# Optimization experiments

Measured on AMD Instinct MI355X. Metric: run time of the kernel, lower is better.

Reference implementation:

```python
import jax, jax.numpy as jnp
import numpy as np

N_HEAD, D_K, D_V, D_MODEL, D_OUT = 8, 64, 64, 512, 512
TOP_K = 5 + 1  # Sparse_attention.__init__ does top_k += 1
EPS = 1e-7
TEMPERATURE = float(np.power(D_K, 0.5))


def setup_inputs() -> dict:
    key = jax.random.key(0)
    ks = jax.random.split(key, 13)
    B, LQ, LK = 4, 1024, 1024
    f32 = jnp.float32
    std_qk = float(np.sqrt(2.0 / (D_MODEL + D_K)))
    std_v = float(np.sqrt(2.0 / (D_MODEL + D_V)))
    std_fc = float(np.sqrt(2.0 / (N_HEAD * D_V + D_OUT)))  # xavier normal
    return {
        "q": jax.random.normal(ks[0], (B, LQ, D_MODEL), f32),
        "k": jax.random.normal(ks[1], (B, LK, D_MODEL), f32),
        "v": jax.random.normal(ks[2], (B, LK, D_MODEL), f32),
        "Wq": jax.random.normal(ks[3], (N_HEAD * D_K, D_MODEL), f32) * std_qk,
        "bq": jax.random.normal(ks[4], (N_HEAD * D_K,), f32) * 0.01,
        "Wk": jax.random.normal(ks[5], (N_HEAD * D_K, D_MODEL), f32) * std_qk,
        "bk": jax.random.normal(ks[6], (N_HEAD * D_K,), f32) * 0.01,
        "Wv": jax.random.normal(ks[7], (N_HEAD * D_V, D_MODEL), f32) * std_v,
        "bv": jax.random.normal(ks[8], (N_HEAD * D_V,), f32) * 0.01,
        "Wfc": jax.random.normal(ks[9], (D_OUT, N_HEAD * D_V), f32) * std_fc,
        "bfc": jax.random.normal(ks[10], (D_OUT,), f32) * 0.01,
        "Wg": jaxax_norm if False else jax.random.normal(ks[11], (D_OUT, N_HEAD * D_V), f32) * std_fc,
        "bg": jax.random.normal(ks[12], (D_OUT,), f32) * 0.01,
    }


def _sparse_attention(attn):
    # attn: (bh, lq, lk) softmax weights; keep values >= TOP_K-th largest per row
    # (time_step = lk > TOP_K always here, so only the else-branch applies)
    delta = jax.lax.top_k(attn, TOP_K)[0][..., -1:] + EPS  # (bh, lq, 1)
    w = jnp.maximum(attn - delta, 0.0)
    return w / (jnp.sum(w, axis=-1, keepdims=True) + EPS)


def reference(q, k, v, Wq, bq, Wk, bk, Wv, bv, Wfc, bfc, Wg, bg):
    B, LQ, _ = q.shape
    LK = k.shape[1]
    # QKV projections, split heads, head-major flatten (matches permute(2,0,1,3))
    qh = (q @ Wq.T + bq).reshape(B, LQ, N_HEAD, D_K)
    kh = (k @ Wk.T + bk).reshape(B, LK, N_HEAD, D_K)
    vh = (v @ Wv.T + bv).reshape(B, LK, N_HEAD, D_V)
    qh = jnp.transpose(qh, (2, 0, 1, 3)).reshape(N_HEAD * B, LQ, D_K)
    kh = jnp.transpose(kh, (2, 0, 1, 3)).reshape(N_HEAD * B, LK, D_K)
    vh = jnp.transpose(vh, (2, 0, 1, 3)).reshape(N_HEAD * B, LK, D_V)
    scores = jnp.einsum("bqd,bkd->bqk", qh, kh) / TEMPERATURE
    attn = jax.nn.softmax(scores, axis=-1)
    attn = _sparse_attention(attn)
    out = jnp.einsum("bqk,bkd->bqd", attn, vh)  # (h*B, lq, d_v)
    out = out.reshape(N_HEAD, B, LQ, D_V)
    out = jnp.transpose(out, (1, 2, 0, 3)).reshape(B, LQ, N_HEAD * D_V)
    # dropout is identity in eval mode
    fc_out = out @ Wfc.T + bfc
    gate = jax.nn.sigmoid(out @ Wg.T + bg)
    output = gate * jnp.tanh(fc_out)
    return output, attn
```

## Files before the change

kernel.cpp:

```cpp
#include <hip/hip_runtime.h>
#include <hip/hip_bf16.h>
#include <math.h>

#define SEQ    1024
#define DMODEL 512
#define OUT0   2097152
#define SP_EPS 1e-7f
#define INV_T  0.125f

typedef __attribute__((ext_vector_type(8))) short bf16x8;
typedef __attribute__((ext_vector_type(4))) float f32x4;

__device__ __forceinline__ unsigned short f2bf(float f) {
  unsigned int b = __float_as_uint(f);
  return (unsigned short)((b + 0x7fffu + ((b >> 16) & 1u)) >> 16);
}
__device__ __forceinline__ float bf2f(unsigned short u) {
  return __uint_as_float(((unsigned int)u) << 16);
}

__device__ __forceinline__ float wred_max(float v) {
#pragma unroll
  for (int o = 32; o > 0; o >>= 1) v = fmaxf(v, __shfl_xor(v, o));
  return v;
}
__device__ __forceinline__ float wred_sum(float v) {
#pragma unroll
  for (int o = 32; o > 0; o >>= 1) v += __shfl_xor(v, o);
  return v;
}

__global__ __launch_bounds__(256) void convW_kernel(
    const float* __restrict__ w0, const float* __restrict__ w1,
    const float* __restrict__ w2, unsigned short* __restrict__ dst)
{
  const int z = blockIdx.z;
  const float* src = (z == 0) ? w0 : (z == 1) ? w1 : w2;
  unsigned short* hi = dst + (size_t)z * (1u << 19);
  unsigned short* lo = hi + (1u << 18);
  const int i = (blockIdx.x * 256 + threadIdx.x) * 4;
  const float4 x = *(const float4*)(src + i);
  ushort4 h, l;
  h.x = f2bf(x.x); l.x = f2bf(x.x - bf2f(h.x));
  h.y = f2bf(x.y); l.y = f2bf(x.y - bf2f(h.y));
  h.z = f2bf(x.z); l.z = f2bf(x.z - bf2f(h.z));
  h.w = f2bf(x.w); l.w = f2bf(x.w - bf2f(h.w));
  *(ushort4*)(hi + i) = h;
  *(ushort4*)(lo + i) = l;
}

__global__ __launch_bounds__(256) void qkv_mfma_kernel(
    const float* __restrict__ q, const float* __restrict__ k, const float* __restrict__ v,
    const unsigned short* __restrict__ Wsplit,
    const float* __restrict__ bq, const float* __restrict__ bk, const float* __restrict__ bv,
    unsigned short* __restrict__ qhh, unsigned short* __restrict__ qhl,
    unsigned short* __restrict__ khh, unsigned short* __restrict__ khl,
    float* __restrict__ vh)
{
  __shared__ short Ash[64 * 64], Asl[64 * 64];
  __shared__ short Bsh[128 * 64], Bsl[128 * 64];
  const int z = blockIdx.z;
  const float* A = (z == 0) ? q : (z == 1) ? k : v;
  const unsigned short* Wh = Wsplit + (size_t)z * (1u << 19);
  const unsigned short* Wl = Wh + (1u << 18);
  const float* bias = (z == 0) ? bq : (z == 1) ? bk : bv;
  const int r0 = blockIdx.x * 64, n0 = blockIdx.y * 128;
  const int tid = threadIdx.x, lane = tid & 63, w = tid >> 6;
  const int wr = w >> 1, wc = w & 1;
  const int l15 = lane & 15, l4 = lane >> 4;

  f32x4 acc[2][4];
#pragma unroll
  for (int a = 0; a < 2; ++a)
#pragma unroll
    for (int b = 0; b < 4; ++b) acc[a][b] = (f32x4){0.f, 0.f, 0.f, 0.f};

  for (int kt = 0; kt < 8; ++kt) {
    __syncthreads();
#pragma unroll
    for (int p = 0; p < 2; ++p) {
      const int c = tid + p * 256, row = c >> 3, k8 = (c & 7) * 8;
      const float4 x0 = *(const float4*)(A + (size_t)(r0 + row) * 512 + kt * 64 + k8);
      const float4 x1 = *(const float4*)(A + (size_t)(r0 + row) * 512 + kt * 64 + k8 + 4);
      bf16x8 hv, lv;
      const float xs[8] = {x0.x, x0.y, x0.z, x0.w, x1.x, x1.y, x1.z, x1.w};
#pragma unroll
      for (int j = 0; j < 8; ++j) {
        const unsigned short h = f2bf(xs[j]);
        hv[j] = (short)h; lv[j] = (short)f2bf(xs[j] - bf2f(h));
      }
      const int si = row * 64 + (k8 ^ ((row & 7) << 3));
      *(bf16x8*)&Ash[si] = hv; *(bf16x8*)&Asl[si] = lv;
    }
#pragma unroll
    for (int p = 0; p < 4; ++p) {
      const int c = tid + p * 256, row = c >> 3, k8 = (c & 7) * 8;
      const size_t go = (size_t)(n0 + row) * 512 + kt * 64 + k8;
      const int si = row * 64 + (k8 ^ ((row & 7) << 3));
      *(bf16x8*)&Bsh[si] = *(const bf16x8*)(Wh + go);
      *(bf16x8*)&Bsl[si] = *(const bf16x8*)(Wl + go);
    }
    __syncthreads();
#pragma unroll
    for (int kf = 0; kf < 2; ++kf) {
      const int kb = kf * 32 + l4 * 8;
      bf16x8 ah[2], al2[2];
#pragma unroll
      for (int rb = 0; rb < 2; ++rb) {
        const int ar = wr * 32 + rb * 16 + l15;
        const int si = ar * 64 + (kb ^ ((ar & 7) << 3));
        ah[rb] = *(bf16x8*)&Ash[si]; al2[rb] = *(bf16x8*)&Asl[si];
      }
#pragma unroll
      for (int cb = 0; cb < 4; ++cb) {
        const int br = wc * 64 + cb * 16 + l15;
        const int si = br * 64 + (kb ^ ((br & 7) << 3));
        const bf16x8 bh = *(bf16x8*)&Bsh[si];
        const bf16x8 bl = *(bf16x8*)&Bsl[si];
#pragma unroll
        for (int rb = 0; rb < 2; ++rb) {
          acc[rb][cb] = __builtin_amdgcn_mfma_f32_16x16x32_bf16(al2[rb], bh, acc[rb][cb], 0, 0, 0);
          acc[rb][cb] = __builtin_amdgcn_mfma_f32_16x16x32_bf16(ah[rb], bl, acc[rb][cb], 0, 0, 0);
          acc[rb][cb] = __builtin_amdgcn_mfma_f32_16x16x32_bf16(ah[rb], bh, acc[rb][cb], 0, 0, 0);
        }
      }
    }
  }
  unsigned short* H = (z == 0) ? qhh : khh;
  unsigned short* L = (z == 0) ? qhl : khl;
#pragma unroll
  for (int cb = 0; cb < 4; ++cb) {
    const int col = n0 + wc * 64 + cb * 16 + l15;
    const float bia = bias[col];
    const int h = col >> 6, d = col & 63;
#pragma unroll
    for (int rb = 0; rb < 2; ++rb)
#pragma unroll
      for (int ri = 0; ri < 4; ++ri) {
        const int row = r0 + wr * 32 + rb * 16 + l4 * 4 + ri;
        const int b = row >> 10, ll = row & 1023;
        const size_t idx = ((size_t)(h * 4 + b) << 16) + (ll << 6) + d;
        const float val = acc[rb][cb][ri] + bia;
        if (z == 2) {
          vh[idx] = val;
        } else {
          const unsigned short hv = f2bf(val);
          H[idx] = hv;
          L[idx] = f2bf(val - bf2f(hv));
        }
      }
  }
}

__global__ __launch_bounds__(512, 4) void scores_sparse_fused_kernel(
    const unsigned short* __restrict__ qhh, const unsigned short* __restrict__ qhl,
    const unsigned short* __restrict__ khh, const unsigned short* __restrict__ khl,
    const float* __restrict__ vh, float* __restrict__ attn,
    unsigned short* __restrict__ ofhi, unsigned short* __restrict__ oflo)
{
  __shared__ float S[16 * 1028];
  __shared__ float s_w[8][8];
  __shared__ int   s_i[8][8];
  const int bh = blockIdx.y;
  const int r0g = blockIdx.x * 16;
  const int tid = threadIdx.x, lane = tid & 63, w = tid >> 6;
  const int l15 = lane & 15, l4 = lane >> 4;
  const size_t base = (size_t)bh << 16;

  bf16x8 qh8[2], ql8[2];
#pragma unroll
  for (int kf = 0; kf < 2; ++kf) {
    const size_t qa = base + (size_t)(r0g + l15) * 64 + kf * 32 + l4 * 8;
    qh8[kf] = *(const bf16x8*)(qhh + qa);
    ql8[kf] = *(const bf16x8*)(qhl + qa);
  }
#pragma unroll
  for (int cb = 0; cb < 8; ++cb) {
    f32x4 acc = (f32x4){0.f, 0.f, 0.f, 0.f};
    const size_t kr = base + (size_t)(w * 128 + cb * 16 + l15) * 64;
#pragma unroll
    for (int kf = 0; kf < 2; ++kf) {
      const bf16x8 kh8 = *(const bf16x8*)(khh + kr + kf * 32 + l4 * 8);
      const bf16x8 kl8 = *(const bf16x8*)(khl + kr + kf * 32 + l4 * 8);
      acc = __builtin_amdgcn_mfma_f32_16x16x32_bf16(ql8[kf], kh8, acc, 0, 0, 0);
      acc = __builtin_amdgcn_mfma_f32_16x16x32_bf16(qh8[kf], kl8, acc, 0, 0, 0);
      acc = __builtin_amdgcn_mfma_f32_16x16x32_bf16(qh8[kf], kh8, acc, 0, 0, 0);
    }
    const int col = w * 128 + cb * 16 + l15;
#pragma unroll
    for (int ri = 0; ri < 4; ++ri)
      S[(l4 * 4 + ri) * 1028 + col] = acc[ri] * INV_T;
  }
  __syncthreads();

#pragma unroll
  for (int rr = 0; rr < 2; ++rr) {
    const int row_local = 2 * w + rr;
    const int lq = r0g + row_local;
    const float* Sr = S + row_local * 1028;

    float u[16];
    {
      const float4 a0 = *(const float4*)(Sr + lane * 4);
      const float4 a1 = *(const float4*)(Sr + 256 + lane * 4);
      const float4 a2 = *(const float4*)(Sr + 512 + lane * 4);
      const float4 a3 = *(const float4*)(Sr + 768 + lane * 4);
      u[0]=a0.x; u[1]=a0.y; u[2]=a0.z; u[3]=a0.w;
      u[4]=a1.x; u[5]=a1.y; u[6]=a1.z; u[7]=a1.w;
      u[8]=a2.x; u[9]=a2.y; u[10]=a2.z; u[11]=a2.w;
      u[12]=a3.x; u[13]=a3.y; u[14]=a3.z; u[15]=a3.w;
    }

    float m = -1e30f;
#pragma unroll
    for (int j = 0; j < 16; ++j) m = fmaxf(m, u[j]);
    m = wred_max(m);
    float Zl = 0.f;
#pragma unroll
    for (int j = 0; j < 16; ++j) { u[j] = __expf(u[j] - m); Zl += u[j]; }
    const float Z = wred_sum(Zl);

    float t0 = -1e30f, t1 = -1e30f, t2 = -1e30f, t3 = -1e30f, t4 = -1e30f, t5 = -1e30f;
#pragma unroll
    for (int j = 0; j < 16; ++j) {
      float v = u[j], a;
      a = fmaxf(t0, v); v = fminf(t0, v); t0 = a;
      a = fmaxf(t1, v); v = fminf(t1, v); t1 = a;
      a = fmaxf(t2, v); v = fminf(t2, v); t2 = a;
      a = fmaxf(t3, v); v = fminf(t3, v); t3 = a;
      a = fmaxf(t4, v); v = fminf(t4, v); t4 = a;
      t5 = fmaxf(t5, v);
    }
#pragma unroll
    for (int off = 1; off < 64; off <<= 1) {
      const float b0 = __shfl_xor(t0, off), b1 = __shfl_xor(t1, off),
                  b2 = __shfl_xor(t2, off), b3 = __shfl_xor(t3, off),
                  b4 = __shfl_xor(t4, off), b5 = __shfl_xor(t5, off);
      float m0 = fmaxf(t0, b5), m1 = fmaxf(t1, b4), m2 = fmaxf(t2, b3),
            m3 = fmaxf(t3, b2), m4 = fmaxf(t4, b1), m5 = fmaxf(t5, b0);
      float a;
      a = fmaxf(m0, m3); m3 = fminf(m0, m3); m0 = a;
      a = fmaxf(m1, m4); m4 = fminf(m1, m4); m1 = a;
      a = fmaxf(m2, m5); m5 = fminf(m2, m5); m2 = a;
      a = fmaxf(m0, m1); m1 = fminf(m0, m1); m0 = a;
      a = fmaxf(m0, m2); m2 = fminf(m0, m2); m0 = a;
      a = fmaxf(m1, m2); m2 = fminf(m1, m2); m1 = a;
      a = fmaxf(m3, m4); m4 = fminf(m3, m4); m3 = a;
      a = fmaxf(m3, m5); m5 = fminf(m3, m5); m3 = a;
      a = fmaxf(m4, m5); m5 = fminf(m4, m5); m4 = a;
      t0 = m0; t1 = m1; t2 = m2; t3 = m3; t4 = m4; t5 = m5;
    }

    const float du = t5 + SP_EPS * Z;
    float wv16[16], Sl = 0.f;
#pragma unroll
    for (int j = 0; j < 16; ++j) { wv16[j] = fmaxf(u[j] - du, 0.f); Sl += wv16[j]; }
    const float Ssum = wred_sum(Sl);
    const float inv = 1.0f / (Ssum + SP_EPS * Z);
#pragma unroll
    for (int j = 0; j < 16; ++j) wv16[j] *= inv;

    float* rp = attn + (((size_t)(bh << 10) + lq) << 10);
    *(float4*)(rp +       lane * 4) = make_float4(wv16[0],  wv16[1],  wv16[2],  wv16[3]);
    *(float4*)(rp + 256 + lane * 4) = make_float4(wv16[4],  wv16[5],  wv16[6],  wv16[7]);
    *(float4*)(rp + 512 + lane * 4) = make_float4(wv16[8],  wv16[9],  wv16[10], wv16[11]);
    *(float4*)(rp + 768 + lane * 4) = make_float4(wv16[12], wv16[13], wv16[14], wv16[15]);

    int nb = 0;
#pragma unroll
    for (int j = 0; j < 16; ++j) {
      const unsigned long long b = __ballot(wv16[j] > 0.f);
      if (wv16[j] > 0.f) {
        const int pos = nb + __popcll(b & ((1ull << lane) - 1ull));
        if (pos < 8) { s_w[w][pos] = wv16[j]; s_i[w][pos] = (j >> 2) * 256 + lane * 4 + (j & 3); }
      }
      nb += __popcll(b);
    }
    if (nb > 8) nb = 8;

    float acc = 0.f;
    const float* vb = vh + base;
    for (int t = 0; t < nb; ++t)
      acc = fmaf(s_w[w][t], vb[((size_t)s_i[w][t] << 6) + lane], acc);
    const int b_ = bh & 3, h = bh >> 2;
    const int idx = (((b_ << 10) | lq) << 9) + (h << 6) + lane;
    const unsigned short hv = f2bf(acc);
    ofhi[idx] = hv;
    oflo[idx] = f2bf(acc - bf2f(hv));
  }
}

__global__ __launch_bounds__(256) void out_proj_mfma_kernel(
    const unsigned short* __restrict__ ofhi, const unsigned short* __restrict__ oflo,
    const unsigned short* __restrict__ FG,
    const float* __restrict__ bfc, const float* __restrict__ bg,
    float* __restrict__ out)
{
  __shared__ short Ash[64 * 64], Asl[64 * 64];
  __shared__ short Bfh[128 * 64], Bfl[128 * 64];
  __shared__ short Bgh[128 * 64], Bgl[128 * 64];
  const unsigned short* Wfh = FG;
  const unsigned short* Wfl = FG + (1u << 18);
  const unsigned short* Wgh = FG + (1u << 19);
  const unsigned short* Wgl = FG + (1u << 19) + (1u << 18);
  const int r0 = blockIdx.x * 64, n0 = blockIdx.y * 128;
  const int tid = threadIdx.x, lane = tid & 63, w = tid >> 6;
  const int wr = w >> 1, wc = w & 1;
  const int l15 = lane & 15, l4 = lane >> 4;

  f32x4 accf[2][4], accg[2][4];
#pragma unroll
  for (int a = 0; a < 2; ++a)
#pragma unroll
    for (int b = 0; b < 4; ++b) {
      accf[a][b] = (f32x4){0.f, 0.f, 0.f, 0.f};
      accg[a][b] = (f32x4){0.f, 0.f, 0.f, 0.f};
    }

  for (int kt = 0; kt < 8; ++kt) {
    __syncthreads();
#pragma unroll
    for (int p = 0; p < 2; ++p) {
      const int c = tid + p * 256, row = c >> 3, k8 = (c & 7) * 8;
      const size_t go = (size_t)(r0 + row) * 512 + kt * 64 + k8;
      const int si = row * 64 + (k8 ^ ((row & 7) << 3));
      *(bf16x8*)&Ash[si] = *(const bf16x8*)(ofhi + go);
      *(bf16x8*)&Asl[si] = *(const bf16x8*)(oflo + go);
    }
#pragma unroll
    for (int p = 0; p < 4; ++p) {
      const int c = tid + p * 256, row = c >> 3, k8 = (c & 7) * 8;
      const int si = row * 64 + (k8 ^ ((row & 7) << 3));
      const size_t go = (size_t)(n0 + row) * 512 + kt * 64 + k8;
      *(bf16x8*)&Bfh[si] = *(const bf16x8*)(Wfh + go);
      *(bf16x8*)&Bfl[si] = *(const bf16x8*)(Wfl + go);
      *(bf16x8*)&Bgh[si] = *(const bf16x8*)(Wgh + go);
      *(bf16x8*)&Bgl[si] = *(const bf16x8*)(Wgl + go);
    }
    __syncthreads();
#pragma unroll
    for (int kf = 0; kf < 2; ++kf) {
      const int kb = kf * 32 + l4 * 8;
      bf16x8 ah[2], al2[2];
#pragma unroll
      for (int rb = 0; rb < 2; ++rb) {
        const int ar = wr * 32 + rb * 16 + l15;
        const int si = ar * 64 + (kb ^ ((ar & 7) << 3));
        ah[rb] = *(bf16x8*)&Ash[si]; al2[rb] = *(bf16x8*)&Asl[si];
      }
#pragma unroll
      for (int cb = 0; cb < 4; ++cb) {
        const int br = wc * 64 + cb * 16 + l15;
        const int si = br * 64 + (kb ^ ((br & 7) << 3));
        const bf16x8 fh = *(bf16x8*)&Bfh[si];
        const bf16x8 fl = *(bf16x8*)&Bfl[si];
        const bf16x8 gh = *(bf16x8*)&Bgh[si];
        const bf16x8 gl = *(bf16x8*)&Bgl[si];
#pragma unroll
        for (int rb = 0; rb < 2; ++rb) {
          accf[rb][cb] = __builtin_amdgcn_mfma_f32_16x16x32_bf16(al2[rb], fh, accf[rb][cb], 0, 0, 0);
          accf[rb][cb] = __builtin_amdgcn_mfma_f32_16x16x32_bf16(ah[rb], fl, accf[rb][cb], 0, 0, 0);
          accf[rb][cb] = __builtin_amdgcn_mfma_f32_16x16x32_bf16(ah[rb], fh, accf[rb][cb], 0, 0, 0);
          accg[rb][cb] = __builtin_amdgcn_mfma_f32_16x16x32_bf16(al2[rb], gh, accg[rb][cb], 0, 0, 0);
          accg[rb][cb] = __builtin_amdgcn_mfma_f32_16x16x32_bf16(ah[rb], gl, accg[rb][cb], 0, 0, 0);
          accg[rb][cb] = __builtin_amdgcn_mfma_f32_16x16x32_bf16(ah[rb], gh, accg[rb][cb], 0, 0, 0);
        }
      }
    }
  }
#pragma unroll
  for (int cb = 0; cb < 4; ++cb) {
    const int col = n0 + wc * 64 + cb * 16 + l15;
    const float bf4 = bfc[col];
    const float bg4 = bg[col];
#pragma unroll
    for (int rb = 0; rb < 2; ++rb)
#pragma unroll
      for (int ri = 0; ri < 4; ++ri) {
        const int row = r0 + wr * 32 + rb * 16 + l4 * 4 + ri;
        const float f = accf[rb][cb][ri] + bf4;
        const float g = accg[rb][cb][ri] + bg4;
        out[(size_t)row * 512 + col] = tanhf(f) / (1.f + __expf(-g));
      }
  }
}

extern "C" void kernel_launch(void* const* d_in, const int* in_sizes, int n_in,
                              void* d_out, int out_size, void* d_ws, size_t ws_size,
                              hipStream_t stream) {
  const float* q   = (const float*)d_in[0];
  const float* k   = (const float*)d_in[1];
  const float* v   = (const float*)d_in[2];
  const float* Wq  = (const float*)d_in[3];
  const float* bq  = (const float*)d_in[4];
  const float* Wk  = (const float*)d_in[5];
  const float* bk  = (const float*)d_in[6];
  const float* Wv  = (const float*)d_in[7];
  const float* bv  = (const float*)d_in[8];
  const float* Wfc = (const float*)d_in[9];
  const float* bfc = (const float*)d_in[10];
  const float* Wg  = (const float*)d_in[11];
  const float* bg  = (const float*)d_in[12];

  float* out  = (float*)d_out;
  float* attn = out + OUT0;

  unsigned short* qhh = (unsigned short*)d_out;
  unsigned short* qhl = qhh + (1u << 21);

  char* wsb = (char*)d_ws;
  unsigned short* khh   = (unsigned short*)wsb;
  unsigned short* khl   = (unsigned short*)(wsb + (4u << 20));
  float*          vh    = (float*)(wsb + (8u << 20));
  unsigned short* Wqkv  = (unsigned short*)(wsb + (16u << 20));
  unsigned short* ofhi  = (unsigned short*)(wsb + (16u << 20));
  unsigned short* oflo  = (unsigned short*)(wsb + (20u << 20));
  unsigned short* FG    = (unsigned short*)wsb;

  convW_kernel<<<dim3(256, 1, 3), 256, 0, stream>>>(Wq, Wk, Wv, Wqkv);
  qkv_mfma_kernel<<<dim3(64, 4, 3), 256, 0, stream>>>(q, k, v, Wqkv, bq, bk, bv,
                                                      qhh, qhl, khh, khl, vh);
  scores_sparse_fused_kernel<<<dim3(64, 32), 512, 0, stream>>>(qhh, qhl, khh, khl,
                                                               vh, attn, ofhi, oflo);
  convW_kernel<<<dim3(256, 1, 2), 256, 0, stream>>>(Wfc, Wg, Wg, FG);
  out_proj_mfma_kernel<<<dim3(64, 4), 256, 0, stream>>>(ofhi, oflo, FG, bfc, bg, out);
}
```

Measured before the change: 156.4 us.

## Stream K tiles twice with online softmax/top-k, scatter sparse attn after zero-fill

Replaces the full-row shared-memory score buffer with a two-pass streaming scheme. The first pass computes online max, sum and a per-lane top-6 over double-buffered, swizzled K tiles in LDS. The second pass recomputes the scores to emit only the surviving weights and their indices. The dense attn output is now written by a separate zero-fill kernel plus sparse scatter writes, which drops the per-row exp/threshold stores from the attention kernel. The cost is doubled QK MFMA work, an extra full-buffer fill pass, and the assumption that at most 5 entries per row survive.

```diff
diff --git a/kernel.cpp b/kernel.cpp
--- a/kernel.cpp
+++ b/kernel.cpp
@@ -2,11 +2,9 @@
 #include <hip/hip_bf16.h>
 #include <math.h>
 
-#define SEQ    1024
-#define DMODEL 512
 #define OUT0   2097152
 #define SP_EPS 1e-7f
-#define INV_T  0.125f
+#define CEXP   0.18033688011112042f
 
 typedef __attribute__((ext_vector_type(8))) short bf16x8;
 typedef __attribute__((ext_vector_type(4))) float f32x4;
@@ -19,15 +17,10 @@
   return __uint_as_float(((unsigned int)u) << 16);
 }
 
-__device__ __forceinline__ float wred_max(float v) {
-#pragma unroll
-  for (int o = 32; o > 0; o >>= 1) v = fmaxf(v, __shfl_xor(v, o));
-  return v;
-}
-__device__ __forceinline__ float wred_sum(float v) {
-#pragma unroll
-  for (int o = 32; o > 0; o >>= 1) v += __shfl_xor(v, o);
-  return v;
+__global__ __launch_bounds__(256) void zerofill_kernel(float4* __restrict__ p, int n4) {
+  const int stride = gridDim.x * 256;
+  for (int i = blockIdx.x * 256 + threadIdx.x; i < n4; i += stride)
+    p[i] = make_float4(0.f, 0.f, 0.f, 0.f);
 }
 
 __global__ __launch_bounds__(256) void convW_kernel(
@@ -152,141 +145,212 @@
   }
 }
 
-__global__ __launch_bounds__(512, 4) void scores_sparse_fused_kernel(
+__global__ __launch_bounds__(256) void sparse_attn_kernel(
     const unsigned short* __restrict__ qhh, const unsigned short* __restrict__ qhl,
     const unsigned short* __restrict__ khh, const unsigned short* __restrict__ khl,
     const float* __restrict__ vh, float* __restrict__ attn,
     unsigned short* __restrict__ ofhi, unsigned short* __restrict__ oflo)
 {
-  __shared__ float S[16 * 1028];
-  __shared__ float s_w[8][8];
-  __shared__ int   s_i[8][8];
+  __shared__ short Kh[2][16 * 64], Kl[2][16 * 64];
+  __shared__ float s_w[4][16][8];
+  __shared__ int   s_i[4][16][8];
+  __shared__ int   s_n[4][16];
   const int bh = blockIdx.y;
-  const int r0g = blockIdx.x * 16;
-  const int tid = threadIdx.x, lane = tid & 63, w = tid >> 6;
+  const int r0 = blockIdx.x * 64;
+  const int tid = threadIdx.x, lane = tid & 63, wvid = tid >> 6;
   const int l15 = lane & 15, l4 = lane >> 4;
   const size_t base = (size_t)bh << 16;
 
   bf16x8 qh8[2], ql8[2];
 #pragma unroll
   for (int kf = 0; kf < 2; ++kf) {
-    const size_t qa = base + (size_t)(r0g + l15) * 64 + kf * 32 + l4 * 8;
+    const size_t qa = base + (size_t)(r0 + wvid * 16 + l15) * 64 + kf * 32 + l4 * 8;
     qh8[kf] = *(const bf16x8*)(qhh + qa);
     ql8[kf] = *(const bf16x8*)(qhl + qa);
   }
-#pragma unroll
-  for (int cb = 0; cb < 8; ++cb) {
+
+  const int s_which = tid >> 7;
+  const int s_rem = tid & 127;
+  const int s_row = s_rem >> 3, s_k8 = (s_rem & 7) * 8;
+  const int s_si = s_row * 64 + (s_k8 ^ ((s_row & 7) << 3));
+  const unsigned short* s_src = (s_which ? khl : khh) + base + s_row * 64 + s_k8;
+
+  const int si0 = l15 * 64 + ((l4 * 8) ^ ((l15 & 7) << 3));
+  const int si1 = l15 * 64 + ((32 + l4 * 8) ^ ((l15 & 7) << 3));
+
+  float m0 = -3e38f, m1 = -3e38f, m2 = -3e38f, m3 = -3e38f;
+  float Z0 = 0.f, Z1 = 0.f, Z2 = 0.f, Z3 = 0.f;
+  float t[4][6];
+#pragma unroll
+  for (int ri = 0; ri < 4; ++ri)
+#pragma unroll
+    for (int j = 0; j < 6; ++j) t[ri][j] = -3e38f;
+
+  { const bf16x8 v0 = *(const bf16x8*)s_src;
+    if (s_which) *(bf16x8*)&Kl[0][s_si] = v0; else *(bf16x8*)&Kh[0][s_si] = v0; }
+
+  for (int kt = 0; kt < 64; ++kt) {
+    __syncthreads();
+    const int cur = kt & 1;
+    bf16x8 nxt;
+    if (kt < 63) nxt = *(const bf16x8*)(s_src + (kt + 1) * 1024);
     f32x4 acc = (f32x4){0.f, 0.f, 0.f, 0.f};
-    const size_t kr = base + (size_t)(w * 128 + cb * 16 + l15) * 64;
 #pragma unroll
     for (int kf = 0; kf < 2; ++kf) {
-      const bf16x8 kh8 = *(const bf16x8*)(khh + kr + kf * 32 + l4 * 8);
-      const bf16x8 kl8 = *(const bf16x8*)(khl + kr + kf * 32 + l4 * 8);
+      const int si = kf ? si1 : si0;
+      const bf16x8 kh8 = *(bf16x8*)&Kh[cur][si];
+      const bf16x8 kl8 = *(bf16x8*)&Kl[cur][si];
       acc = __builtin_amdgcn_mfma_f32_16x16x32_bf16(ql8[kf], kh8, acc, 0, 0, 0);
       acc = __builtin_amdgcn_mfma_f32_16x16x32_bf16(qh8[kf], kl8, acc, 0, 0, 0);
       acc = __builtin_amdgcn_mfma_f32_16x16x32_bf16(qh8[kf], kh8, acc, 0, 0, 0);
     }
-    const int col = w * 128 + cb * 16 + l15;
-#pragma unroll
-    for (int ri = 0; ri < 4; ++ri)
-      S[(l4 * 4 + ri) * 1028 + col] = acc[ri] * INV_T;
-  }
-  __syncthreads();
-
-#pragma unroll
-  for (int rr = 0; rr < 2; ++rr) {
-    const int row_local = 2 * w + rr;
-    const int lq = r0g + row_local;
-    const float* Sr = S + row_local * 1028;
-
-    float u[16];
-    {
-      const float4 a0 = *(const float4*)(Sr + lane * 4);
-      const float4 a1 = *(const float4*)(Sr + 256 + lane * 4);
-      const float4 a2 = *(const float4*)(Sr + 512 + lane * 4);
-      const float4 a3 = *(const float4*)(Sr + 768 + lane * 4);
-      u[0]=a0.x; u[1]=a0.y; u[2]=a0.z; u[3]=a0.w;
-      u[4]=a1.x; u[5]=a1.y; u[6]=a1.z; u[7]=a1.w;
-      u[8]=a2.x; u[9]=a2.y; u[10]=a2.z; u[11]=a2.w;
-      u[12]=a3.x; u[13]=a3.y; u[14]=a3.z; u[15]=a3.w;
-    }
-
-    float m = -1e30f;
-#pragma unroll
-    for (int j = 0; j < 16; ++j) m = fmaxf(m, u[j]);
-    m = wred_max(m);
-    float Zl = 0.f;
-#pragma unroll
-    for (int j = 0; j < 16; ++j) { u[j] = __expf(u[j] - m); Zl += u[j]; }
-    const float Z = wred_sum(Zl);
-
-    float t0 = -1e30f, t1 = -1e30f, t2 = -1e30f, t3 = -1e30f, t4 = -1e30f, t5 = -1e30f;
-#pragma unroll
-    for (int j = 0; j < 16; ++j) {
-      float v = u[j], a;
-      a = fmaxf(t0, v); v = fminf(t0, v); t0 = a;
-      a = fmaxf(t1, v); v = fminf(t1, v); t1 = a;
-      a = fmaxf(t2, v); v = fminf(t2, v); t2 = a;
-      a = fmaxf(t3, v); v = fminf(t3, v); t3 = a;
-      a = fmaxf(t4, v); v = fminf(t4, v); t4 = a;
-      t5 = fmaxf(t5, v);
-    }
-#pragma unroll
-    for (int off = 1; off < 64; off <<= 1) {
+#pragma unroll
+    for (int ri = 0; ri < 4; ++ri) {
+      const float d = acc[ri];
+      float* mp = (ri == 0) ? &m0 : (ri == 1) ? &m1 : (ri == 2) ? &m2 : &m3;
+      float* zp = (ri == 0) ? &Z0 : (ri == 1) ? &Z1 : (ri == 2) ? &Z2 : &Z3;
+      const float nm = fmaxf(*mp, d);
+      *zp = *zp * exp2f((*mp - nm) * CEXP) + exp2f((d - nm) * CEXP);
+      *mp = nm;
+      float v = d;
+#pragma unroll
+      for (int j = 0; j < 6; ++j) {
+        const float a = fmaxf(t[ri][j], v);
+        v = fminf(t[ri][j], v);
+        t[ri][j] = a;
+      }
+    }
+    if (kt < 63) {
+      if (s_which) *(bf16x8*)&Kl[cur ^ 1][s_si] = nxt;
+      else         *(bf16x8*)&Kh[cur ^ 1][s_si] = nxt;
+    }
+  }
+
+  float mC[4], u6p[4], inv[4], Zm[4];
+  float mA[4] = {m0, m1, m2, m3};
+  float ZA[4] = {Z0, Z1, Z2, Z3};
+#pragma unroll
+  for (int ri = 0; ri < 4; ++ri) {
+    const float ml = mA[ri];
+    float mg = ml;
+#pragma unroll
+    for (int off = 1; off < 16; off <<= 1) mg = fmaxf(mg, __shfl_xor(mg, off));
+    float zz = ZA[ri] * exp2f((ml - mg) * CEXP);
+#pragma unroll
+    for (int off = 1; off < 16; off <<= 1) zz += __shfl_xor(zz, off);
+    float t0 = t[ri][0], t1 = t[ri][1], t2 = t[ri][2],
+          t3 = t[ri][3], t4 = t[ri][4], t5 = t[ri][5];
+#pragma unroll
+    for (int off = 1; off < 16; off <<= 1) {
       const float b0 = __shfl_xor(t0, off), b1 = __shfl_xor(t1, off),
                   b2 = __shfl_xor(t2, off), b3 = __shfl_xor(t3, off),
                   b4 = __shfl_xor(t4, off), b5 = __shfl_xor(t5, off);
-      float m0 = fmaxf(t0, b5), m1 = fmaxf(t1, b4), m2 = fmaxf(t2, b3),
-            m3 = fmaxf(t3, b2), m4 = fmaxf(t4, b1), m5 = fmaxf(t5, b0);
+      float n0 = fmaxf(t0, b5), n1 = fmaxf(t1, b4), n2 = fmaxf(t2, b3),
+            n3 = fmaxf(t3, b2), n4 = fmaxf(t4, b1), n5 = fmaxf(t5, b0);
       float a;
-      a = fmaxf(m0, m3); m3 = fminf(m0, m3); m0 = a;
-      a = fmaxf(m1, m4); m4 = fminf(m1, m4); m1 = a;
-      a = fmaxf(m2, m5); m5 = fminf(m2, m5); m2 = a;
-      a = fmaxf(m0, m1); m1 = fminf(m0, m1); m0 = a;
-      a = fmaxf(m0, m2); m2 = fminf(m0, m2); m0 = a;
-      a = fmaxf(m1, m2); m2 = fminf(m1, m2); m1 = a;
-      a = fmaxf(m3, m4); m4 = fminf(m3, m4); m3 = a;
-      a = fmaxf(m3, m5); m5 = fminf(m3, m5); m3 = a;
-      a = fmaxf(m4, m5); m5 = fminf(m4, m5); m4 = a;
-      t0 = m0; t1 = m1; t2 = m2; t3 = m3; t4 = m4; t5 = m5;
-    }
-
-    const float du = t5 + SP_EPS * Z;
-    float wv16[16], Sl = 0.f;
-#pragma unroll
-    for (int j = 0; j < 16; ++j) { wv16[j] = fmaxf(u[j] - du, 0.f); Sl += wv16[j]; }
-    const float Ssum = wred_sum(Sl);
-    const float inv = 1.0f / (Ssum + SP_EPS * Z);
-#pragma unroll
-    for (int j = 0; j < 16; ++j) wv16[j] *= inv;
-
-    float* rp = attn + (((size_t)(bh << 10) + lq) << 10);
-    *(float4*)(rp +       lane * 4) = make_float4(wv16[0],  wv16[1],  wv16[2],  wv16[3]);
-    *(float4*)(rp + 256 + lane * 4) = make_float4(wv16[4],  wv16[5],  wv16[6],  wv16[7]);
-    *(float4*)(rp + 512 + lane * 4) = make_float4(wv16[8],  wv16[9],  wv16[10], wv16[11]);
-    *(float4*)(rp + 768 + lane * 4) = make_float4(wv16[12], wv16[13], wv16[14], wv16[15]);
-
-    int nb = 0;
-#pragma unroll
-    for (int j = 0; j < 16; ++j) {
-      const unsigned long long b = __ballot(wv16[j] > 0.f);
-      if (wv16[j] > 0.f) {
-        const int pos = nb + __popcll(b & ((1ull << lane) - 1ull));
-        if (pos < 8) { s_w[w][pos] = wv16[j]; s_i[w][pos] = (j >> 2) * 256 + lane * 4 + (j & 3); }
-      }
-      nb += __popcll(b);
-    }
-    if (nb > 8) nb = 8;
-
-    float acc = 0.f;
-    const float* vb = vh + base;
-    for (int t = 0; t < nb; ++t)
-      acc = fmaf(s_w[w][t], vb[((size_t)s_i[w][t] << 6) + lane], acc);
-    const int b_ = bh & 3, h = bh >> 2;
+      a = fmaxf(n0, n3); n3 = fminf(n0, n3); n0 = a;
+      a = fmaxf(n1, n4); n4 = fminf(n1, n4); n1 = a;
+      a = fmaxf(n2, n5); n5 = fminf(n2, n5); n2 = a;
+      a = fmaxf(n0, n1); n1 = fminf(n0, n1); n0 = a;
+      a = fmaxf(n0, n2); n2 = fminf(n0, n2); n0 = a;
+      a = fmaxf(n1, n2); n2 = fminf(n1, n2); n1 = a;
+      a = fmaxf(n3, n4); n4 = fminf(n3, n4); n3 = a;
+      a = fmaxf(n3, n5); n5 = fminf(n3, n5); n3 = a;
+      a = fmaxf(n4, n5); n5 = fminf(n4, n5); n4 = a;
+      t0 = n0; t1 = n1; t2 = n2; t3 = n3; t4 = n4; t5 = n5;
+    }
+    const float mCg = mg * CEXP;
+    const float u6 = exp2f(fmaf(t5, CEXP, -mCg));
+    const float u6x = u6 + SP_EPS * zz;
+    float Ss = 0.f;
+    Ss += fmaxf(exp2f(fmaf(t0, CEXP, -mCg)) - u6x, 0.f);
+    Ss += fmaxf(exp2f(fmaf(t1, CEXP, -mCg)) - u6x, 0.f);
+    Ss += fmaxf(exp2f(fmaf(t2, CEXP, -mCg)) - u6x, 0.f);
+    Ss += fmaxf(exp2f(fmaf(t3, CEXP, -mCg)) - u6x, 0.f);
+    Ss += fmaxf(exp2f(fmaf(t4, CEXP, -mCg)) - u6x, 0.f);
+    mC[ri] = mCg; u6p[ri] = u6x; Zm[ri] = zz;
+    inv[ri] = 1.0f / (Ss + SP_EPS * zz);
+  }
+
+  {
+    float* pw = &s_w[wvid][0][0];
+    int*   pi = &s_i[wvid][0][0];
+    pw[lane] = 0.f; pw[lane + 64] = 0.f;
+    pi[lane] = 0;   pi[lane + 64] = 0;
+  }
+
+  int cnt[4] = {0, 0, 0, 0};
+  { const bf16x8 v0 = *(const bf16x8*)s_src;
+    if (s_which) *(bf16x8*)&Kl[0][s_si] = v0; else *(bf16x8*)&Kh[0][s_si] = v0; }
+
+  for (int kt = 0; kt < 64; ++kt) {
+    __syncthreads();
+    const int cur = kt & 1;
+    bf16x8 nxt;
+    if (kt < 63) nxt = *(const bf16x8*)(s_src + (kt + 1) * 1024);
+    f32x4 acc = (f32x4){0.f, 0.f, 0.f, 0.f};
+#pragma unroll
+    for (int kf = 0; kf < 2; ++kf) {
+      const int si = kf ? si1 : si0;
+      const bf16x8 kh8 = *(bf16x8*)&Kh[cur][si];
+      const bf16x8 kl8 = *(bf16x8*)&Kl[cur][si];
+      acc = __builtin_amdgcn_mfma_f32_16x16x32_bf16(ql8[kf], kh8, acc, 0, 0, 0);
+      acc = __builtin_amdgcn_mfma_f32_16x16x32_bf16(qh8[kf], kl8, acc, 0, 0, 0);
+      acc = __builtin_amdgcn_mfma_f32_16x16x32_bf16(qh8[kf], kh8, acc, 0, 0, 0);
+    }
+#pragma unroll
+    for (int ri = 0; ri < 4; ++ri) {
+      const float u = exp2f(fmaf(acc[ri], CEXP, -mC[ri]));
+      const float wv = u - u6p[ri];
+      const unsigned long long mask = __ballot(wv > 0.f);
+      if (mask) {
+        const unsigned sub = (unsigned)(mask >> (l4 * 16)) & 0xFFFFu;
+        if (sub) {
+          if (wv > 0.f) {
+            const int pos = cnt[ri] + __popc(sub & ((1u << l15) - 1u));
+            if (pos < 8) {
+              s_w[wvid][l4 * 4 + ri][pos] = wv * inv[ri];
+              s_i[wvid][l4 * 4 + ri][pos] = kt * 16 + l15;
+            }
+          }
+          cnt[ri] += __popc(sub);
+        }
+      }
+    }
+    if (kt < 63) {
+      if (s_which) *(bf16x8*)&Kl[cur ^ 1][s_si] = nxt;
+      else         *(bf16x8*)&Kh[cur ^ 1][s_si] = nxt;
+    }
+  }
+
+  if (l15 == 0) {
+#pragma unroll
+    for (int ri = 0; ri < 4; ++ri) s_n[wvid][l4 * 4 + ri] = cnt[ri];
+  }
+
+  float accv[16];
+#pragma unroll
+  for (int r = 0; r < 16; ++r) accv[r] = 0.f;
+  const float* vb = vh + base;
+  float* arow = attn + ((size_t)bh << 20) + ((size_t)(r0 + wvid * 16) << 10);
+#pragma unroll
+  for (int tt = 0; tt < 5; ++tt) {
+#pragma unroll
+    for (int r = 0; r < 16; ++r) {
+      const float wgt = s_w[wvid][r][tt];
+      const int kvi = s_i[wvid][r][tt];
+      accv[r] = fmaf(wgt, vb[(size_t)kvi * 64 + lane], accv[r]);
+      if (lane == 0 && wgt > 0.f) arow[(size_t)r * 1024 + kvi] = wgt;
+    }
+  }
+  const int b_ = bh & 3, h = bh >> 2;
+#pragma unroll
+  for (int r = 0; r < 16; ++r) {
+    const int lq = r0 + wvid * 16 + r;
     const int idx = (((b_ << 10) | lq) << 9) + (h << 6) + lane;
-    const unsigned short hv = f2bf(acc);
+    const unsigned short hv = f2bf(accv[r]);
     ofhi[idx] = hv;
-    oflo[idx] = f2bf(acc - bf2f(hv));
+    oflo[idx] = f2bf(accv[r] - bf2f(hv));
   }
 }
 
@@ -301,8 +365,8 @@
   __shared__ short Bgh[128 * 64], Bgl[128 * 64];
   const unsigned short* Wfh = FG;
   const unsigned short* Wfl = FG + (1u << 18);
-  const unsigned short* Wgh = FG + (1u << 19);
-  const unsigned short* Wgl = FG + (1u << 19) + (1u << 18);
+  const unsigned short* Wgh = FG + (2u << 18);
+  const unsigned short* Wgl = FG + 3u * (1u << 18);
   const int r0 = blockIdx.x * 64, n0 = blockIdx.y * 128;
   const int tid = threadIdx.x, lane = tid & 63, w = tid >> 6;
   const int wr = w >> 1, wc = w & 1;
@@ -409,19 +473,20 @@
   unsigned short* qhl = qhh + (1u << 21);
 
   char* wsb = (char*)d_ws;
-  unsigned short* khh   = (unsigned short*)wsb;
-  unsigned short* khl   = (unsigned short*)(wsb + (4u << 20));
-  float*          vh    = (float*)(wsb + (8u << 20));
-  unsigned short* Wqkv  = (unsigned short*)(wsb + (16u << 20));
-  unsigned short* ofhi  = (unsigned short*)(wsb + (16u << 20));
-  unsigned short* oflo  = (unsigned short*)(wsb + (20u << 20));
-  unsigned short* FG    = (unsigned short*)wsb;
-
+  unsigned short* khh  = (unsigned short*)wsb;
+  unsigned short* khl  = (unsigned short*)(wsb + (4u << 20));
+  float*          vh   = (float*)(wsb + (8u << 20));
+  unsigned short* Wqkv = (unsigned short*)(wsb + (16u << 20));
+  unsigned short* ofhi = (unsigned short*)(wsb + (16u << 20));
+  unsigned short* oflo = (unsigned short*)(wsb + (20u << 20));
+  unsigned short* FG   = (unsigned short*)wsb;
+
+  zerofill_kernel<<<dim3(2048), 256, 0, stream>>>((float4*)attn, 1 << 23);
   convW_kernel<<<dim3(256, 1, 3), 256, 0, stream>>>(Wq, Wk, Wv, Wqkv);
   qkv_mfma_kernel<<<dim3(64, 4, 3), 256, 0, stream>>>(q, k, v, Wqkv, bq, bk, bv,
                                                       qhh, qhl, khh, khl, vh);
-  scores_sparse_fused_kernel<<<dim3(64, 32), 512, 0, stream>>>(qhh, qhl, khh, khl,
-                                                               vh, attn, ofhi, oflo);
+  sparse_attn_kernel<<<dim3(16, 32), 256, 0, stream>>>(qhh, qhl, khh, khl, vh,
+                                                       attn, ofhi, oflo);
   convW_kernel<<<dim3(256, 1, 2), 256, 0, stream>>>(Wfc, Wg, Wg, FG);
   out_proj_mfma_kernel<<<dim3(64, 4), 256, 0, stream>>>(ofhi, oflo, FG, bfc, bg, out);
 }
```

Result: slower. 174.7 us (+11.7%).
